# Optimization experiments

Hardware: AMD Instinct MI355X
Metric: run time of the kernel (lower is better)

## Reference

```python
import jax, jax.numpy as jnp
import numpy as np

B, S, E, H = 4, 2048, 1024, 16
D = E // H  # head_dim = 64


def setup_inputs() -> dict:
    key = jax.random.key(0)
    ks = jax.random.split(key, 5)
    return {
        "x": jax.random.normal(ks[0], (B, S, E), dtype=jnp.float32),
        "w_qkv": jax.random.normal(ks[1], (3 * E, E), dtype=jnp.float32) * (E ** -0.5),
        "b_qkv": jax.random.normal(ks[2], (3 * E,), dtype=jnp.float32) * 0.02,
        "w_proj": jax.random.normal(ks[3], (E, E), dtype=jnp.float32) * (E ** -0.5),
        "b_proj": jax.random.normal(ks[4], (E,), dtype=jnp.float32) * 0.02,
    }


def reference(x, w_qkv, b_qkv, w_proj, b_proj):
    # fused QKV projection: [B,S,E] -> [B,S,3E] -> [B,S,3,H,D]
    qkv = (jnp.einsum("bse,fe->bsf", x, w_qkv) + b_qkv).reshape(B, S, 3, H, D)
    q, k, v = qkv[:, :, 0], qkv[:, :, 1], qkv[:, :, 2]  # each [B,S,H,D]
    scale = 1.0 / jnp.sqrt(jnp.asarray(D, dtype=q.dtype))
    scores = jnp.einsum("bqhd,bkhd->bhqk", q, k) * scale  # [B,H,S,S]
    attn = jax.nn.softmax(scores, axis=-1)
    out = jnp.einsum("bhqk,bkhd->bqhd", attn, v).reshape(B, S, E)
    return jnp.einsum("bse,fe->bsf", out, w_proj) + b_proj
```

## Files before the change

### kernel.cpp

```cpp
#include <hip/hip_runtime.h>
#include <cstdint>
#include <cstddef>

#define B_ 4
#define S_ 2048
#define E_ 1024
#define H_ 16
#define D_ 64
#define M_ (B_*S_)
#define NE_ ((size_t)B_*H_*S_*D_)

typedef unsigned int  u32;
typedef unsigned short u16;
typedef __attribute__((ext_vector_type(8))) short bf16x8;
typedef __attribute__((ext_vector_type(4))) float f32x4;

__device__ __forceinline__ u16 f2bf(float x) {
    u32 u = __float_as_uint(x);
    u32 r = (u + 0x7FFFu + ((u >> 16) & 1u)) >> 16;
    return (u16)r;
}
__device__ __forceinline__ float bf2f(u16 h) { return __uint_as_float((u32)h << 16); }

__device__ __forceinline__ void gload_lds16(const void* gsrc, void* lds) {
    __builtin_amdgcn_global_load_lds(
        (const __attribute__((address_space(1))) u32*)gsrc,
        (__attribute__((address_space(3))) u32*)lds, 16, 0, 0);
}


__global__ __launch_bounds__(256)
void convert_img(const float* __restrict__ src, u16* __restrict__ dh, u16* __restrict__ dl)
{
    const int tile = blockIdx.x;
    const int nt = tile >> 4, kt = tile & 15;
    const size_t tb = (size_t)tile << 12;
    #pragma unroll
    for (int u = 0; u < 2; ++u) {
        const int ci = threadIdx.x + u * 256;
        const int r  = ci >> 3;
        const int c  = ci & 7;
        const float* s = src + ((size_t)(nt * 64 + r)) * 1024 + kt * 64 + c * 8;
        const float4 f0 = *(const float4*)s;
        const float4 f1 = *(const float4*)(s + 4);
        const float vals[8] = {f0.x, f0.y, f0.z, f0.w, f1.x, f1.y, f1.z, f1.w};
        __align__(16) short hs[8];
        __align__(16) short ls[8];
        #pragma unroll
        for (int j = 0; j < 8; ++j) {
            const u16 h = f2bf(vals[j]);
            hs[j] = (short)h;
            ls[j] = (short)f2bf(vals[j] - bf2f(h));
        }
        const size_t eoff = tb + r * 64 + ((size_t)(c ^ (r & 7)) << 3);
        *(bf16x8*)(dh + eoff) = *(const bf16x8*)hs;
        *(bf16x8*)(dl + eoff) = *(const bf16x8*)ls;
    }
}

template<int MODE>
__global__ __launch_bounds__(256)
void gemm_mfma(const u16* __restrict__ AIh, const u16* __restrict__ AIl,
               const u16* __restrict__ BIh, const u16* __restrict__ BIl,
               const float* __restrict__ bias, float* __restrict__ Cout,
               u16* __restrict__ qh, u16* __restrict__ ql,
               u16* __restrict__ kh,
               u16* __restrict__ vh, u16* __restrict__ vl)
{
    __shared__ __align__(16) u16 sA[2][2][4096];
    __shared__ __align__(16) u16 sB[2][2][4096];

    const int tid = threadIdx.x, lane = tid & 63, w = tid >> 6;
    const int quad = lane >> 4, l15 = lane & 15;
    const int m0  = blockIdx.x * 128;
    const int n0  = blockIdx.y * 128;
    const int mt0 = blockIdx.x * 2;
    const int nt0 = blockIdx.y * 2;
    const int rw  = w >> 1;
    const int cw  = w & 1;

    const int isB = w >> 1;
    const int sbw = w & 1;

    f32x4 acc[4][4];
    #pragma unroll
    for (int i = 0; i < 4; ++i)
        #pragma unroll
        for (int j = 0; j < 4; ++j)
            acc[i][j] = (f32x4){0.f, 0.f, 0.f, 0.f};

    for (int kt = 0; kt < 16; ++kt) {
        __syncthreads();
        {
            const size_t atile = ((size_t)((mt0 + sbw) * 16 + kt)) << 12;
            const size_t btile = ((size_t)((nt0 + sbw) * 16 + kt)) << 12;
            const u16* srcH = isB ? (BIh + btile) : (AIh + atile);
            const u16* srcL = isB ? (BIl + btile) : (AIl + atile);
            u16* dstH = isB ? &sB[sbw][0][0] : &sA[sbw][0][0];
            u16* dstL = isB ? &sB[sbw][1][0] : &sA[sbw][1][0];
            #pragma unroll
            for (int it = 0; it < 8; ++it)
                gload_lds16(srcH + it * 512 + lane * 8, dstH + it * 512);
            #pragma unroll
            for (int it = 0; it < 8; ++it)
                gload_lds16(srcL + it * 512 + lane * 8, dstL + it * 512);
        }
        __syncthreads();

        #pragma unroll
        for (int kk = 0; kk < 2; ++kk) {
            bf16x8 aH[4], aL[4], bH[4], bL[4];
            #pragma unroll
            for (int i = 0; i < 4; ++i) {
                const int r = i * 16 + l15;
                const int off = r * 64 + (((kk * 4 + quad) ^ (r & 7)) << 3);
                aH[i] = *(const bf16x8*)&sA[rw][0][off];
                aL[i] = *(const bf16x8*)&sA[rw][1][off];
            }
            #pragma unroll
            for (int j = 0; j < 4; ++j) {
                const int r = j * 16 + l15;
                const int off = r * 64 + (((kk * 4 + quad) ^ (r & 7)) << 3);
                bH[j] = *(const bf16x8*)&sB[cw][0][off];
                bL[j] = *(const bf16x8*)&sB[cw][1][off];
            }
            #pragma unroll
            for (int i = 0; i < 4; ++i)
                #pragma unroll
                for (int j = 0; j < 4; ++j) {
                    acc[i][j] = __builtin_amdgcn_mfma_f32_16x16x32_bf16(aL[i], bH[j], acc[i][j], 0, 0, 0);
                    acc[i][j] = __builtin_amdgcn_mfma_f32_16x16x32_bf16(aH[i], bL[j], acc[i][j], 0, 0, 0);
                    acc[i][j] = __builtin_amdgcn_mfma_f32_16x16x32_bf16(aH[i], bH[j], acc[i][j], 0, 0, 0);
                }
        }
    }

    const int fbase = n0 + cw * 64;
    float bj[4];
    #pragma unroll
    for (int j = 0; j < 4; ++j) bj[j] = bias[fbase + j * 16 + l15];

    if (MODE == 0) {
        const int cR = fbase >> 10;
        const int hh = (fbase >> 6) & 15;
        #pragma unroll
        for (int i = 0; i < 4; ++i)
            #pragma unroll
            for (int j = 0; j < 4; ++j)
                #pragma unroll
                for (int reg = 0; reg < 4; ++reg) {
                    float val = acc[i][j][reg] + bj[j];
                    const int m = m0 + rw * 64 + i * 16 + quad * 4 + reg;
                    const int d = j * 16 + l15;
                    const int bb = m >> 11, s = m & 2047;
                    const int bh = bb * 16 + hh;
                    if (cR == 0) val *= 0.125f;
                    const u16 h = f2bf(val);
                    if (cR == 0) {
                        const u16 lo = f2bf(val - bf2f(h));
                        const size_t idx = ((size_t)bh * 2048 + s) * 64 + d;
                        qh[idx] = h; ql[idx] = lo;
                    } else if (cR == 1) {
                        const size_t tile = (size_t)bh * 32 + (s >> 6);
                        const int r = s & 63;
                        const size_t off = (tile << 12) + r * 64 + (((d >> 3) ^ (r & 7)) << 3) + (d & 7);
                        kh[off] = h;
                    } else {
                        const u16 lo = f2bf(val - bf2f(h));
                        const size_t tile = (size_t)bh * 32 + (s >> 6);
                        const size_t off = (tile << 12) + d * 64 + ((((s & 63) >> 3) ^ (d & 7)) << 3) + (s & 7);
                        vh[off] = h; vl[off] = lo;
                    }
                }
    } else {
        #pragma unroll
        for (int i = 0; i < 4; ++i)
            #pragma unroll
            for (int j = 0; j < 4; ++j)
                #pragma unroll
                for (int reg = 0; reg < 4; ++reg) {
                    const int m = m0 + rw * 64 + i * 16 + quad * 4 + reg;
                    const int f = fbase + j * 16 + l15;
                    Cout[(size_t)m * 1024 + f] = acc[i][j][reg] + bj[j];
                }
    }
}

__global__ __launch_bounds__(256, 3)
void attn_mfma(const u16* __restrict__ qh, const u16* __restrict__ ql,
               const u16* __restrict__ kh,
               const u16* __restrict__ vh, const u16* __restrict__ vl,
               u16* __restrict__ oh, u16* __restrict__ ol)
{
    __shared__ __align__(16) u16 KV[3][4096];
    __shared__ __align__(16) u16 Psh[4][2304];

    const int tid  = threadIdx.x;
    const int lane = tid & 63, w = tid >> 6;
    const int quad = lane >> 4, l15 = lane & 15;
    const int bh = blockIdx.y;
    const int q0 = blockIdx.x * 128 + w * 32;

    bf16x8 Qf[2][2][2];
    #pragma unroll
    for (int qs = 0; qs < 2; ++qs)
        #pragma unroll
        for (int kk = 0; kk < 2; ++kk) {
            const size_t idx = ((size_t)bh * S_ + q0 + qs * 16 + l15) * 64 + kk * 32 + quad * 8;
            Qf[qs][kk][0] = *(const bf16x8*)(qh + idx);
            Qf[qs][kk][1] = *(const bf16x8*)(ql + idx);
        }

    f32x4 O[2][4];
    float l_part[2][4];
    #pragma unroll
    for (int qs = 0; qs < 2; ++qs)
        #pragma unroll
        for (int r = 0; r < 4; ++r) l_part[qs][r] = 0.f;
    #pragma unroll
    for (int qs = 0; qs < 2; ++qs)
        #pragma unroll
        for (int ds = 0; ds < 4; ++ds)
            O[qs][ds] = (f32x4){0.f, 0.f, 0.f, 0.f};

    const char* gk[3] = {(const char*)kh, (const char*)vh, (const char*)vl};

    for (int kt = 0; kt < S_ / 64; ++kt) {
        __syncthreads();
        const size_t tb = (((size_t)bh * 32 + kt) << 13);
        #pragma unroll
        for (int a = 0; a < 3; ++a)
            #pragma unroll
            for (int it = 0; it < 2; ++it) {
                const int off = w * 2048 + it * 1024;
                gload_lds16(gk[a] + tb + off + lane * 16, (char*)&KV[a][0] + off);
            }
        __syncthreads();

        f32x4 S[2][4];
        #pragma unroll
        for (int qs = 0; qs < 2; ++qs)
            #pragma unroll
            for (int ks = 0; ks < 4; ++ks)
                S[qs][ks] = (f32x4){-16.f, -16.f, -16.f, -16.f};

        #pragma unroll
        for (int ks = 0; ks < 4; ++ks) {
            const int r = ks * 16 + l15;
            #pragma unroll
            for (int kk = 0; kk < 2; ++kk) {
                const int c = (kk * 4 + quad) ^ (r & 7);
                const bf16x8 Kh = *(const bf16x8*)&KV[0][r * 64 + c * 8];
                #pragma unroll
                for (int qs = 0; qs < 2; ++qs) {
                    S[qs][ks] = __builtin_amdgcn_mfma_f32_16x16x32_bf16(Qf[qs][kk][1], Kh, S[qs][ks], 0, 0, 0);
                    S[qs][ks] = __builtin_amdgcn_mfma_f32_16x16x32_bf16(Qf[qs][kk][0], Kh, S[qs][ks], 0, 0, 0);
                }
            }
        }

        #pragma unroll
        for (int qs = 0; qs < 2; ++qs)
            #pragma unroll
            for (int reg = 0; reg < 4; ++reg) {
                float p[4];
                p[0] = __expf(S[qs][0][reg]);
                p[1] = __expf(S[qs][1][reg]);
                p[2] = __expf(S[qs][2][reg]);
                p[3] = __expf(S[qs][3][reg]);
                l_part[qs][reg] += (p[0] + p[1]) + (p[2] + p[3]);
                const int qloc = qs * 16 + quad * 4 + reg;
                #pragma unroll
                for (int ks = 0; ks < 4; ++ks)
                    Psh[w][qloc * 72 + ks * 16 + l15] = f2bf(p[ks]);
            }

        #pragma unroll
        for (int kk = 0; kk < 2; ++kk) {
            bf16x8 PhF[2];
            #pragma unroll
            for (int qs = 0; qs < 2; ++qs) {
                const int pidx = (qs * 16 + l15) * 72 + kk * 32 + quad * 8;
                PhF[qs] = *(const bf16x8*)&Psh[w][pidx];
            }
            #pragma unroll
            for (int ds = 0; ds < 4; ++ds) {
                const int r = ds * 16 + l15;
                const int c = (kk * 4 + quad) ^ (r & 7);
                const bf16x8 Vh = *(const bf16x8*)&KV[1][r * 64 + c * 8];
                const bf16x8 Vl = *(const bf16x8*)&KV[2][r * 64 + c * 8];
                #pragma unroll
                for (int qs = 0; qs < 2; ++qs) {
                    O[qs][ds] = __builtin_amdgcn_mfma_f32_16x16x32_bf16(PhF[qs], Vl, O[qs][ds], 0, 0, 0);
                    O[qs][ds] = __builtin_amdgcn_mfma_f32_16x16x32_bf16(PhF[qs], Vh, O[qs][ds], 0, 0, 0);
                }
            }
        }
    }

    #pragma unroll
    for (int qs = 0; qs < 2; ++qs)
        #pragma unroll
        for (int reg = 0; reg < 4; ++reg) {
            float rs = l_part[qs][reg];
            rs += __shfl_xor(rs, 1, 16);
            rs += __shfl_xor(rs, 2, 16);
            rs += __shfl_xor(rs, 4, 16);
            rs += __shfl_xor(rs, 8, 16);
            l_part[qs][reg] = 1.f / rs;
        }

    const int bb = bh >> 4, hh = bh & 15;
    #pragma unroll
    for (int qs = 0; qs < 2; ++qs)
        #pragma unroll
        for (int reg = 0; reg < 4; ++reg) {
            const float inv = l_part[qs][reg];
            const int s = q0 + qs * 16 + quad * 4 + reg;
            const int m = bb * 2048 + s;
            const int mt = m >> 6, r = m & 63;
            const size_t tbase = ((size_t)(mt * 16 + hh)) << 12;
            #pragma unroll
            for (int ds = 0; ds < 4; ++ds) {
                const int d = ds * 16 + l15;
                const float val = O[qs][ds][reg] * inv;
                const u16 h  = f2bf(val);
                const u16 lo = f2bf(val - bf2f(h));
                const size_t off = tbase + r * 64 + (((d >> 3) ^ (r & 7)) << 3) + (d & 7);
                oh[off] = h; ol[off] = lo;
            }
        }
}

extern "C" void kernel_launch(void* const* d_in, const int* in_sizes, int n_in,
                              void* d_out, int out_size, void* d_ws, size_t ws_size,
                              hipStream_t stream) {
    const float* x      = (const float*)d_in[0];
    const float* w_qkv  = (const float*)d_in[1];
    const float* b_qkv  = (const float*)d_in[2];
    const float* w_proj = (const float*)d_in[3];
    const float* b_proj = (const float*)d_in[4];
    float* out = (float*)d_out;

    u16* qh  = (u16*)d_ws;
    u16* ql  = qh + NE_;
    u16* kh  = ql + NE_;
    u16* vh  = kh + NE_;
    u16* vl  = vh + NE_;
    u16* xh  = vl + NE_;
    u16* xl  = xh + NE_;
    u16* wqh = xl + NE_;
    u16* wql = wqh + (size_t)3 * 1024 * 1024;
    u16* oh  = xh;
    u16* ol  = xl;
    u16* wph = wqh;
    u16* wpl = wph + (size_t)1024 * 1024;

    convert_img<<<(M_ / 64) * 16, 256, 0, stream>>>(x, xh, xl);
    convert_img<<<48 * 16, 256, 0, stream>>>(w_qkv, wqh, wql);

    {
        dim3 grid(M_ / 128, (3 * E_) / 128);
        gemm_mfma<0><<<grid, 256, 0, stream>>>(xh, xl, wqh, wql,
                                               b_qkv, nullptr, qh, ql, kh, vh, vl);
    }
    {
        dim3 grid(S_ / 128, B_ * H_);
        attn_mfma<<<grid, 256, 0, stream>>>(qh, ql, kh, vh, vl, oh, ol);
    }
    convert_img<<<16 * 16, 256, 0, stream>>>(w_proj, wph, wpl);
    {
        dim3 grid(M_ / 128, E_ / 128);
        gemm_mfma<1><<<grid, 256, 0, stream>>>(oh, ol, wph, wpl,
                                               b_proj, out, nullptr, nullptr, nullptr,
                                               nullptr, nullptr);
    }
}
```

Baseline: 446.8 us.

## Enlarge attention blocks to 512 threads, transpose S MFMA, use exp2 softmax

The attention kernel now runs 8 waves per block covering 256 queries, so each K/V tile loaded into LDS is shared by twice as many waves and each wave issues one load per array instead of two. The QK^T MFMA operands are swapped so each lane holds four keys for a single query. This allows packed 64-bit stores of P, and the row sums need only two cross-lane shuffles. Q is prescaled by log2(e)/8 and exp2f replaces __expf, with a matching fixed max offset. The trade-off is larger LDS use per block and a different occupancy limit under the new launch bounds.

New measurement: 465.4 us. 4.2% more time.

```diff
diff --git a/kernel.cpp b/kernel.cpp
--- a/kernel.cpp
+++ b/kernel.cpp
@@ -9,6 +9,9 @@
 #define D_ 64
 #define M_ (B_*S_)
 #define NE_ ((size_t)B_*H_*S_*D_)
+
+#define QSCALE 0.18033688011112042f
+#define SINIT  -23.083120654223414f
 
 typedef unsigned int  u32;
 typedef unsigned short u16;
@@ -78,7 +81,6 @@
     const int nt0 = blockIdx.y * 2;
     const int rw  = w >> 1;
     const int cw  = w & 1;
-
     const int isB = w >> 1;
     const int sbw = w & 1;
 
@@ -154,7 +156,7 @@
                     const int d = j * 16 + l15;
                     const int bb = m >> 11, s = m & 2047;
                     const int bh = bb * 16 + hh;
-                    if (cR == 0) val *= 0.125f;
+                    if (cR == 0) val *= QSCALE;
                     const u16 h = f2bf(val);
                     if (cR == 0) {
                         const u16 lo = f2bf(val - bf2f(h));
@@ -186,20 +188,20 @@
     }
 }
 
-__global__ __launch_bounds__(256, 3)
+__global__ __launch_bounds__(512, 4)
 void attn_mfma(const u16* __restrict__ qh, const u16* __restrict__ ql,
                const u16* __restrict__ kh,
                const u16* __restrict__ vh, const u16* __restrict__ vl,
                u16* __restrict__ oh, u16* __restrict__ ol)
 {
     __shared__ __align__(16) u16 KV[3][4096];
-    __shared__ __align__(16) u16 Psh[4][2304];
+    __shared__ __align__(16) u16 Psh[8][2304];
 
     const int tid  = threadIdx.x;
     const int lane = tid & 63, w = tid >> 6;
     const int quad = lane >> 4, l15 = lane & 15;
     const int bh = blockIdx.y;
-    const int q0 = blockIdx.x * 128 + w * 32;
+    const int q0 = blockIdx.x * 256 + w * 32;
 
     bf16x8 Qf[2][2][2];
     #pragma unroll
@@ -212,11 +214,7 @@
         }
 
     f32x4 O[2][4];
-    float l_part[2][4];
-    #pragma unroll
-    for (int qs = 0; qs < 2; ++qs)
-        #pragma unroll
-        for (int r = 0; r < 4; ++r) l_part[qs][r] = 0.f;
+    float l_lane[2] = {0.f, 0.f};
     #pragma unroll
     for (int qs = 0; qs < 2; ++qs)
         #pragma unroll
@@ -230,49 +228,44 @@
         const size_t tb = (((size_t)bh * 32 + kt) << 13);
         #pragma unroll
         for (int a = 0; a < 3; ++a)
-            #pragma unroll
-            for (int it = 0; it < 2; ++it) {
-                const int off = w * 2048 + it * 1024;
-                gload_lds16(gk[a] + tb + off + lane * 16, (char*)&KV[a][0] + off);
-            }
+            gload_lds16(gk[a] + tb + w * 1024 + lane * 16, (char*)&KV[a][0] + w * 1024);
         __syncthreads();
 
-        f32x4 S[2][4];
-        #pragma unroll
-        for (int qs = 0; qs < 2; ++qs)
-            #pragma unroll
-            for (int ks = 0; ks < 4; ++ks)
-                S[qs][ks] = (f32x4){-16.f, -16.f, -16.f, -16.f};
-
-        #pragma unroll
-        for (int ks = 0; ks < 4; ++ks) {
-            const int r = ks * 16 + l15;
+        f32x4 ST[4][2];
+        #pragma unroll
+        for (int kst = 0; kst < 4; ++kst)
+            #pragma unroll
+            for (int qs = 0; qs < 2; ++qs)
+                ST[kst][qs] = (f32x4){SINIT, SINIT, SINIT, SINIT};
+
+        #pragma unroll
+        for (int kst = 0; kst < 4; ++kst) {
+            const int r = kst * 16 + l15;
             #pragma unroll
             for (int kk = 0; kk < 2; ++kk) {
                 const int c = (kk * 4 + quad) ^ (r & 7);
                 const bf16x8 Kh = *(const bf16x8*)&KV[0][r * 64 + c * 8];
                 #pragma unroll
                 for (int qs = 0; qs < 2; ++qs) {
-                    S[qs][ks] = __builtin_amdgcn_mfma_f32_16x16x32_bf16(Qf[qs][kk][1], Kh, S[qs][ks], 0, 0, 0);
-                    S[qs][ks] = __builtin_amdgcn_mfma_f32_16x16x32_bf16(Qf[qs][kk][0], Kh, S[qs][ks], 0, 0, 0);
-                }
-            }
-        }
-
-        #pragma unroll
-        for (int qs = 0; qs < 2; ++qs)
-            #pragma unroll
-            for (int reg = 0; reg < 4; ++reg) {
+                    ST[kst][qs] = __builtin_amdgcn_mfma_f32_16x16x32_bf16(Kh, Qf[qs][kk][1], ST[kst][qs], 0, 0, 0);
+                    ST[kst][qs] = __builtin_amdgcn_mfma_f32_16x16x32_bf16(Kh, Qf[qs][kk][0], ST[kst][qs], 0, 0, 0);
+                }
+            }
+        }
+
+        #pragma unroll
+        for (int kst = 0; kst < 4; ++kst)
+            #pragma unroll
+            for (int qs = 0; qs < 2; ++qs) {
                 float p[4];
-                p[0] = __expf(S[qs][0][reg]);
-                p[1] = __expf(S[qs][1][reg]);
-                p[2] = __expf(S[qs][2][reg]);
-                p[3] = __expf(S[qs][3][reg]);
-                l_part[qs][reg] += (p[0] + p[1]) + (p[2] + p[3]);
-                const int qloc = qs * 16 + quad * 4 + reg;
-                #pragma unroll
-                for (int ks = 0; ks < 4; ++ks)
-                    Psh[w][qloc * 72 + ks * 16 + l15] = f2bf(p[ks]);
+                #pragma unroll
+                for (int reg = 0; reg < 4; ++reg)
+                    p[reg] = exp2f(ST[kst][qs][reg]);
+                l_lane[qs] += (p[0] + p[1]) + (p[2] + p[3]);
+                uint2 pk;
+                pk.x = (u32)f2bf(p[0]) | ((u32)f2bf(p[1]) << 16);
+                pk.y = (u32)f2bf(p[2]) | ((u32)f2bf(p[3]) << 16);
+                *(uint2*)&Psh[w][(qs * 16 + l15) * 72 + kst * 16 + quad * 4] = pk;
             }
 
         #pragma unroll
@@ -298,24 +291,21 @@
         }
     }
 
+    float linv[2];
+    #pragma unroll
+    for (int qs = 0; qs < 2; ++qs) {
+        float rs = l_lane[qs];
+        rs += __shfl_xor(rs, 16);
+        rs += __shfl_xor(rs, 32);
+        linv[qs] = 1.f / rs;
+    }
+
+    const int bb = bh >> 4, hh = bh & 15;
     #pragma unroll
     for (int qs = 0; qs < 2; ++qs)
         #pragma unroll
         for (int reg = 0; reg < 4; ++reg) {
-            float rs = l_part[qs][reg];
-            rs += __shfl_xor(rs, 1, 16);
-            rs += __shfl_xor(rs, 2, 16);
-            rs += __shfl_xor(rs, 4, 16);
-            rs += __shfl_xor(rs, 8, 16);
-            l_part[qs][reg] = 1.f / rs;
-        }
-
-    const int bb = bh >> 4, hh = bh & 15;
-    #pragma unroll
-    for (int qs = 0; qs < 2; ++qs)
-        #pragma unroll
-        for (int reg = 0; reg < 4; ++reg) {
-            const float inv = l_part[qs][reg];
+            const float inv = __shfl(linv[qs], quad * 4 + reg, 16);
             const int s = q0 + qs * 16 + quad * 4 + reg;
             const int m = bb * 2048 + s;
             const int mt = m >> 6, r = m & 63;
@@ -365,8 +355,8 @@
                                                b_qkv, nullptr, qh, ql, kh, vh, vl);
     }
     {
-        dim3 grid(S_ / 128, B_ * H_);
-        attn_mfma<<<grid, 256, 0, stream>>>(qh, ql, kh, vh, vl, oh, ol);
+        dim3 grid(S_ / 256, B_ * H_);
+        attn_mfma<<<grid, 512, 0, stream>>>(qh, ql, kh, vh, vl, oh, ol);
     }
     convert_img<<<16 * 16, 256, 0, stream>>>(w_proj, wph, wpl);
     {
```
